# Kernel tuning notes

Measured on AMD Instinct MI355X. Metric: run time of the kernel, lower is better.

## Reference

```python
import jax, jax.numpy as jnp
import numpy as np

NEG_SLOPE = 0.2  # PyG GATConv default leaky_relu slope
BN_EPS = 1e-5


def gat_conv(x, src, dst, num_nodes, W, a_src, a_dst, bias, concat):
    """PyG-style GATConv (eval mode, self-loops already appended to src/dst)."""
    H, F = a_src.shape
    h = (x @ W).reshape(num_nodes, H, F)              # [N,H,F]
    e_src = jnp.einsum('nhf,hf->nh', h, a_src)        # [N,H]
    e_dst = jnp.einsum('nhf,hf->nh', h, a_dst)        # [N,H]
    e = jax.nn.leaky_relu(e_src[src] + e_dst[dst], NEG_SLOPE)  # [E,H]
    m = jax.ops.segment_max(e, dst, num_segments=num_nodes)    # segment softmax (stable)
    w = jnp.exp(e - m[dst])
    z = jax.ops.segment_sum(w, dst, num_segments=num_nodes)
    alpha = w / (z[dst] + 1e-16)                      # [E,H]
    msg = alpha[:, :, None] * h[src]                  # [E,H,F]
    out = jax.ops.segment_sum(msg, dst, num_segments=num_nodes)  # [N,H,F]
    out = out.reshape(num_nodes, H * F) if concat else out.mean(axis=1)
    return out + bias


def bn_eval(x, gamma, beta):
    # BatchNorm1d eval with initialized running stats (mean=0, var=1)
    return x * (gamma / jnp.sqrt(1.0 + BN_EPS)) + beta


def setup_inputs() -> dict:
    key = jax.random.key(0)
    ks = jax.random.split(key, 16)
    N, E, Fin, H, Fh, MLP = 50000, 800000, 128, 4, 32, 64
    HF = H * Fh  # 128
    s = 0.05
    inp = {
        'x': jax.random.normal(ks[0], (N, Fin), jnp.float32),
        'edge_index': jax.random.randint(ks[1], (2, E), 0, N, jnp.int64),
        # conv0: Fin -> Fh per head, concat
        'W1': jax.random.normal(ks[2], (Fin, HF), jnp.float32) * s,
        'a1s': jax.random.normal(ks[3], (H, Fh), jnp.float32) * s,
        'a1d': jax.random.normal(ks[4], (H, Fh), jnp.float32) * s,
        'b1': jnp.zeros((HF,), jnp.float32),
        # conv1: HF -> Fh per head, concat
        'W2': jax.random.normal(ks[5], (HF, HF), jnp.float32) * s,
        'a2s': jax.random.normal(ks[6], (H, Fh), jnp.float32) * s,
        'a2d': jax.random.normal(ks[7], (H, Fh), jnp.float32) * s,
        'b2': jnp.zeros((HF,), jnp.float32),
        # mlp block 0
        'M1w': jax.random.normal(ks[8], (HF, MLP), jnp.float32) * s,
        'M1b': jnp.zeros((MLP,), jnp.float32),
        'g1': jnp.ones((MLP,), jnp.float32),
        'be1': jnp.zeros((MLP,), jnp.float32),
        'M2w': jax.random.normal(ks[9], (MLP, HF), jnp.float32) * s,
        'M2b': jnp.zeros((HF,), jnp.float32),
        'g2': jnp.ones((HF,), jnp.float32),
        'be2': jnp.zeros((HF,), jnp.float32),
        # conv2: HF -> Fh per head, mean over heads (concat=False)
        'W3': jax.random.normal(ks[10], (HF, HF), jnp.float32) * s,
        'a3s': jax.random.normal(ks[11], (H, Fh), jnp.float32) * s,
        'a3d': jax.random.normal(ks[12], (H, Fh), jnp.float32) * s,
        'b3': jnp.zeros((Fh,), jnp.float32),
    }
    return inp


def reference(x, edge_index, W1, a1s, a1d, b1, W2, a2s, a2d, b2,
              M1w, M1b, g1, be1, M2w, M2b, g2, be2, W3, a3s, a3d, b3):
    N = x.shape[0]
    loops = jnp.arange(N, dtype=edge_index.dtype)
    src = jnp.concatenate([edge_index[0], loops])  # add self-loops (PyG default)
    dst = jnp.concatenate([edge_index[1], loops])

    # layer 0: conv -> relu -> (dropout=id, eval) -> mlp[0]
    h = jax.nn.relu(gat_conv(x, src, dst, N, W1, a1s, a1d, b1, concat=True))
    h = bn_eval(jax.nn.relu(h @ M1w + M1b), g1, be1)
    h = bn_eval(jax.nn.relu(h @ M2w + M2b), g2, be2)

    # layer 1: conv -> relu -> (dropout=id)
    h = jax.nn.relu(gat_conv(h, src, dst, N, W2, a2s, a2d, b2, concat=True))

    # output layer: concat=False -> mean over heads
    out = gat_conv(h, src, dst, N, W3, a3s, a3d, b3, concat=False)
    return out
```

## Files before the change

### kernel.cpp

```cpp
#include <hip/hip_runtime.h>
#include <hip/hip_bf16.h>

#define NEG_SLOPE 0.2f
#define BN_RS 0.9999950000374997f

typedef __attribute__((ext_vector_type(8))) _Float16 f16x8;
typedef __attribute__((ext_vector_type(2))) _Float16 f16x2;
typedef __attribute__((ext_vector_type(4))) float f32x4;

__device__ __forceinline__ void store_split(float w, _Float16* H, _Float16* L, size_t off) {
  _Float16 h = (_Float16)w;
  H[off] = h;
  L[off] = (_Float16)(w - (float)h);
}


__global__ void zero256(int* p) { p[threadIdx.x] = 0; }

__global__ void eb_hist(const int* __restrict__ ei, int* __restrict__ bucketSize, int E) {
  __shared__ int h[256];
  int tid = threadIdx.x;
  h[tid] = 0;
  __syncthreads();
  for (int i = blockIdx.x * 256 + tid; i < E; i += gridDim.x * 256)
    atomicAdd(&h[ei[E + i] >> 8], 1);
  __syncthreads();
  if (h[tid]) atomicAdd(&bucketSize[tid], h[tid]);
}

__global__ void eb_scan(const int* __restrict__ bucketSize, int* __restrict__ edgeStart,
                        int* __restrict__ cursor, int* __restrict__ csrStart, int N) {
  __shared__ int sd[256];
  int tid = threadIdx.x;
  int v = bucketSize[tid];
  sd[tid] = v;
  __syncthreads();
  for (int off = 1; off < 256; off <<= 1) {
    int t = (tid >= off) ? sd[tid - off] : 0;
    __syncthreads();
    sd[tid] += t;
    __syncthreads();
  }
  int excl = sd[tid] - v;
  edgeStart[tid] = excl;
  cursor[tid] = excl;
  csrStart[tid] = excl + min(tid << 8, N);
  if (tid == 255) edgeStart[256] = sd[255];
}

#define PCH 4096
__global__ __launch_bounds__(256) void eb_part(const int* __restrict__ ei,
                                               int* __restrict__ cursor,
                                               unsigned* __restrict__ staging, int E) {
  __shared__ unsigned val[PCH];
  __shared__ unsigned char bk[PCH];
  __shared__ int cnt[256];
  __shared__ int base[256];
  int tid = threadIdx.x;
  cnt[tid] = 0;
  __syncthreads();
  int e0 = blockIdx.x * PCH;
  int n = min(PCH, E - e0);
  for (int j = tid; j < n; j += 256) {
    int s = ei[e0 + j], d = ei[E + e0 + j];
    val[j] = ((unsigned)(d & 255) << 16) | (unsigned)s;
    int b = d >> 8;
    bk[j] = (unsigned char)b;
    atomicAdd(&cnt[b], 1);
  }
  __syncthreads();
  if (cnt[tid]) base[tid] = atomicAdd(&cursor[tid], cnt[tid]);
  __syncthreads();
  for (int j = tid; j < n; j += 256) {
    int b = bk[j];
    int off = atomicSub(&cnt[b], 1) - 1;
    staging[base[b] + off] = val[j];
  }
}

__global__ __launch_bounds__(256) void eb_csr(
    const unsigned* __restrict__ staging, const int* __restrict__ edgeStart,
    const int* __restrict__ csrStart, int* __restrict__ rowptr,
    unsigned* __restrict__ csr, int N) {
  __shared__ int deg[256];
  __shared__ int sc[256];
  __shared__ int ex[256];
  int b = blockIdx.x, tid = threadIdx.x;
  int n0 = b << 8;
  int nn = min(256, N - n0);
  deg[tid] = (tid < nn) ? 1 : 0;
  __syncthreads();
  int s0 = edgeStart[b], s1 = edgeStart[b + 1];
  for (int j = s0 + tid; j < s1; j += 256)
    atomicAdd(&deg[staging[j] >> 16], 1);
  __syncthreads();
  int dv = deg[tid];
  sc[tid] = dv;
  __syncthreads();
  for (int off = 1; off < 256; off <<= 1) {
    int t = (tid >= off) ? sc[tid - off] : 0;
    __syncthreads();
    sc[tid] += t;
    __syncthreads();
  }
  int incl = sc[tid];
  int cbase = csrStart[b];
  ex[tid] = incl - dv;
  if (tid < nn) {
    rowptr[n0 + tid + 1] = cbase + incl;
    unsigned me = (unsigned)(n0 + tid);
    csr[cbase + incl - 1] = (me << 16) | me;
  }
  if (b == 0 && tid == 0) rowptr[0] = 0;
  deg[tid] = 0;
  __syncthreads();
  for (int j = s0 + tid; j < s1; j += 256) {
    unsigned v = staging[j];
    int dl = v >> 16;
    unsigned src = v & 0xFFFF;
    int off = atomicAdd(&deg[dl], 1);
    csr[cbase + ex[dl] + off] = ((unsigned)(n0 + dl) << 16) | src;
  }
}

__device__ __forceinline__ void wprep_conv(const float* __restrict__ W,
                                           const float* __restrict__ as_,
                                           const float* __restrict__ ad_,
                                           _Float16* __restrict__ H, _Float16* __restrict__ L,
                                           int lb, int tid) {
  if (lb < 64) {
    int idx = lb * 256 + tid;
    int k = idx >> 7, p = idx & 127;
    store_split(W[k * 128 + p], H, L, (size_t)p * 128 + k);
  } else if (lb < 68) {
    int idx = (lb - 64) * 256 + tid;
    int rl = idx >> 7, k = idx & 127;
    const float* a = (rl < 4) ? as_ : ad_;
    int h = rl & 3;
    float s = 0.f;
#pragma unroll
    for (int f = 0; f < 32; f++) s += W[k * 128 + h * 32 + f] * a[h * 32 + f];
    store_split(s, H, L, (size_t)(128 + rl) * 128 + k);
  } else {
    int idx = (lb - 68) * 256 + tid;
    int rl = idx >> 7, k = idx & 127;
    H[(size_t)(136 + rl) * 128 + k] = (_Float16)0.f;
    L[(size_t)(136 + rl) * 128 + k] = (_Float16)0.f;
  }
}

__global__ void wprep_all(
    const float* __restrict__ W1, const float* __restrict__ a1s, const float* __restrict__ a1d,
    _Float16* __restrict__ W1H, _Float16* __restrict__ W1L,
    const float* __restrict__ W2, const float* __restrict__ a2s, const float* __restrict__ a2d,
    _Float16* __restrict__ W2H, _Float16* __restrict__ W2L,
    const float* __restrict__ W3, const float* __restrict__ a3s, const float* __restrict__ a3d,
    _Float16* __restrict__ W3H, _Float16* __restrict__ W3L,
    const float* __restrict__ M1, _Float16* __restrict__ M1H, _Float16* __restrict__ M1L,
    const float* __restrict__ M2, _Float16* __restrict__ M2H, _Float16* __restrict__ M2L) {
  int b = blockIdx.x, tid = threadIdx.x;
  if (b < 72)       wprep_conv(W1, a1s, a1d, W1H, W1L, b, tid);
  else if (b < 144) wprep_conv(W2, a2s, a2d, W2H, W2L, b - 72, tid);
  else if (b < 216) wprep_conv(W3, a3s, a3d, W3H, W3L, b - 144, tid);
  else if (b < 248) {
    int idx = (b - 216) * 256 + tid;
    int k = idx >> 6, p = idx & 63;
    store_split(M1[k * 64 + p], M1H, M1L, (size_t)p * 128 + k);
  } else {
    int idx = (b - 248) * 256 + tid;
    int k = idx >> 7, p = idx & 127;
    store_split(M2[k * 128 + p], M2H, M2L, (size_t)p * 64 + k);
  }
}

template <typename TA>
__global__ __launch_bounds__(256) void gemm_f16(
    const TA* __restrict__ A, const _Float16* __restrict__ WtH,
    const _Float16* __restrict__ WtL, _Float16* __restrict__ C, int N,
    float* __restrict__ esb, float* __restrict__ edb) {
  constexpr int PT = 144, PST = 128, K = 128;
  constexpr int CTB = 2;
  constexpr int KT = K / 32;
  __shared__ _Float16 As[128 * 32];
  __shared__ _Float16 WsH[PT * 32];
  __shared__ _Float16 WsL[PT * 32];
  const int tid = threadIdx.x;
  const int wave = tid >> 6, lane = tid & 63;
  const int quad = lane >> 4, l16 = lane & 15;
  const int row0 = blockIdx.x * 128;
  const bool xw = (wave == 0);

  f32x4 acc[8][CTB + 1];
#pragma unroll
  for (int rt = 0; rt < 8; rt++)
#pragma unroll
    for (int nt = 0; nt < CTB + 1; nt++) acc[rt][nt] = (f32x4){0.f, 0.f, 0.f, 0.f};

  for (int kc = 0; kc < KT; ++kc) {
    {
      int r = tid >> 1, part = tid & 1;
      int gr = row0 + r;
      _Float16* dst = &As[r * 32 + part * 16];
      if (gr < N) {
        const TA* src = A + (size_t)gr * K + kc * 32 + part * 16;
        if constexpr (sizeof(TA) == 4) {
          f16x8 h0, h1;
#pragma unroll
          for (int j = 0; j < 8; j++) { h0[j] = (_Float16)src[j]; h1[j] = (_Float16)src[8 + j]; }
          *(f16x8*)dst = h0; *(f16x8*)(dst + 8) = h1;
        } else {
          uint4 v0 = *(const uint4*)src;
          uint4 v1 = *(const uint4*)(src + 8);
          *(uint4*)dst = v0; *(uint4*)(dst + 8) = v1;
        }
      } else {
        *(uint4*)dst = make_uint4(0, 0, 0, 0);
        *(uint4*)(dst + 8) = make_uint4(0, 0, 0, 0);
      }
    }
    for (int idx = tid; idx < PT * 2; idx += 256) {
      int isL = idx >= PT;
      int p = isL ? idx - PT : idx;
      const _Float16* src = (isL ? WtL : WtH) + (size_t)p * K + kc * 32;
      _Float16* dst = (isL ? WsL : WsH) + p * 32;
      uint4 a0 = *(const uint4*)src;       uint4 a1 = *(const uint4*)(src + 8);
      uint4 a2 = *(const uint4*)(src + 16); uint4 a3 = *(const uint4*)(src + 24);
      *(uint4*)dst = a0; *(uint4*)(dst + 8) = a1;
      *(uint4*)(dst + 16) = a2; *(uint4*)(dst + 24) = a3;
    }
    __syncthreads();

    f16x8 bh[CTB], bl[CTB], bhE, blE;
#pragma unroll
    for (int nt = 0; nt < CTB; nt++) {
      int p = (wave * CTB + nt) * 16 + l16;
      bh[nt] = *(f16x8*)&WsH[p * 32 + quad * 8];
      bl[nt] = *(f16x8*)&WsL[p * 32 + quad * 8];
    }
    if (xw) {
      int p = 4 * CTB * 16 + l16;
      bhE = *(f16x8*)&WsH[p * 32 + quad * 8];
      blE = *(f16x8*)&WsL[p * 32 + quad * 8];
    }
#pragma unroll
    for (int rt = 0; rt < 8; rt++) {
      f16x8 a = *(f16x8*)&As[(rt * 16 + l16) * 32 + quad * 8];
#pragma unroll
      for (int nt = 0; nt < CTB; nt++) {
        acc[rt][nt] = __builtin_amdgcn_mfma_f32_16x16x32_f16(a, bh[nt], acc[rt][nt], 0, 0, 0);
        acc[rt][nt] = __builtin_amdgcn_mfma_f32_16x16x32_f16(a, bl[nt], acc[rt][nt], 0, 0, 0);
      }
      if (xw) {
        acc[rt][CTB] = __builtin_amdgcn_mfma_f32_16x16x32_f16(a, bhE, acc[rt][CTB], 0, 0, 0);
        acc[rt][CTB] = __builtin_amdgcn_mfma_f32_16x16x32_f16(a, blE, acc[rt][CTB], 0, 0, 0);
      }
    }
    __syncthreads();
  }

#pragma unroll
  for (int nt = 0; nt < CTB; nt++) {
    int c = (wave * CTB + nt) * 16 + l16;
#pragma unroll
    for (int rt = 0; rt < 8; rt++)
#pragma unroll
      for (int g = 0; g < 4; g++) {
        int r = row0 + rt * 16 + quad * 4 + g;
        if (r < N) C[(size_t)r * PST + c] = (_Float16)acc[rt][nt][g];
      }
  }
  if (wave == 0 && l16 < 8) {
    float* dstb = (l16 < 4) ? esb : edb;
    int h = l16 & 3;
#pragma unroll
    for (int rt = 0; rt < 8; rt++)
#pragma unroll
      for (int g = 0; g < 4; g++) {
        int r = row0 + rt * 16 + quad * 4 + g;
        if (r < N) dstb[(size_t)r * 4 + h] = acc[rt][CTB][g];
      }
  }
}

__global__ __launch_bounds__(256) void mlp_fused(
    const _Float16* __restrict__ A,
    const _Float16* __restrict__ M1H, const _Float16* __restrict__ M1L,
    const _Float16* __restrict__ M2H, const _Float16* __restrict__ M2L,
    _Float16* __restrict__ C, int N,
    const float* __restrict__ b1v, const float* __restrict__ g1v, const float* __restrict__ be1v,
    const float* __restrict__ b2v, const float* __restrict__ g2v, const float* __restrict__ be2v) {
  __shared__ _Float16 As[128 * 32];
  __shared__ _Float16 W1Hs[64 * 32], W1Ls[64 * 32];
  __shared__ _Float16 T[128 * 72];
  __shared__ _Float16 W2Hs[128 * 32], W2Ls[128 * 32];
  const int tid = threadIdx.x;
  const int wave = tid >> 6, lane = tid & 63;
  const int quad = lane >> 4, l16 = lane & 15;
  const int row0 = blockIdx.x * 128;

  f32x4 acc1[8];
#pragma unroll
  for (int rt = 0; rt < 8; rt++) acc1[rt] = (f32x4){0.f, 0.f, 0.f, 0.f};
  for (int kc = 0; kc < 4; ++kc) {
    {
      int r = tid >> 1, part = tid & 1;
      int gr = row0 + r;
      _Float16* dst = &As[r * 32 + part * 16];
      if (gr < N) {
        const _Float16* src = A + (size_t)gr * 128 + kc * 32 + part * 16;
        uint4 v0 = *(const uint4*)src;
        uint4 v1 = *(const uint4*)(src + 8);
        *(uint4*)dst = v0; *(uint4*)(dst + 8) = v1;
      } else {
        *(uint4*)dst = make_uint4(0, 0, 0, 0);
        *(uint4*)(dst + 8) = make_uint4(0, 0, 0, 0);
      }
    }
    if (tid < 128) {
      int isL = tid >= 64;
      int p = tid & 63;
      const _Float16* src = (isL ? M1L : M1H) + (size_t)p * 128 + kc * 32;
      _Float16* dst = (isL ? W1Ls : W1Hs) + p * 32;
      uint4 a0 = *(const uint4*)src;       uint4 a1 = *(const uint4*)(src + 8);
      uint4 a2 = *(const uint4*)(src + 16); uint4 a3 = *(const uint4*)(src + 24);
      *(uint4*)dst = a0; *(uint4*)(dst + 8) = a1;
      *(uint4*)(dst + 16) = a2; *(uint4*)(dst + 24) = a3;
    }
    __syncthreads();
    int p = wave * 16 + l16;
    f16x8 bh = *(f16x8*)&W1Hs[p * 32 + quad * 8];
    f16x8 bl = *(f16x8*)&W1Ls[p * 32 + quad * 8];
#pragma unroll
    for (int rt = 0; rt < 8; rt++) {
      f16x8 a = *(f16x8*)&As[(rt * 16 + l16) * 32 + quad * 8];
      acc1[rt] = __builtin_amdgcn_mfma_f32_16x16x32_f16(a, bh, acc1[rt], 0, 0, 0);
      acc1[rt] = __builtin_amdgcn_mfma_f32_16x16x32_f16(a, bl, acc1[rt], 0, 0, 0);
    }
    __syncthreads();
  }
  {
    int c = wave * 16 + l16;
    float bi = b1v[c], ga = g1v[c] * BN_RS, be = be1v[c];
#pragma unroll
    for (int rt = 0; rt < 8; rt++)
#pragma unroll
      for (int g = 0; g < 4; g++) {
        int r = rt * 16 + quad * 4 + g;
        float v = acc1[rt][g] + bi;
        v = v > 0.f ? v : 0.f;
        v = v * ga + be;
        T[r * 72 + c] = (_Float16)v;
      }
  }
  __syncthreads();

  f32x4 acc2[8][2];
#pragma unroll
  for (int rt = 0; rt < 8; rt++)
#pragma unroll
    for (int nt = 0; nt < 2; nt++) acc2[rt][nt] = (f32x4){0.f, 0.f, 0.f, 0.f};
  for (int kc = 0; kc < 2; ++kc) {
    {
      int isL = tid >= 128;
      int p = tid & 127;
      const _Float16* src = (isL ? M2L : M2H) + (size_t)p * 64 + kc * 32;
      _Float16* dst = (isL ? W2Ls : W2Hs) + p * 32;
      uint4 a0 = *(const uint4*)src;       uint4 a1 = *(const uint4*)(src + 8);
      uint4 a2 = *(const uint4*)(src + 16); uint4 a3 = *(const uint4*)(src + 24);
      *(uint4*)dst = a0; *(uint4*)(dst + 8) = a1;
      *(uint4*)(dst + 16) = a2; *(uint4*)(dst + 24) = a3;
    }
    __syncthreads();
    f16x8 bh[2], bl[2];
#pragma unroll
    for (int nt = 0; nt < 2; nt++) {
      int p = (wave * 2 + nt) * 16 + l16;
      bh[nt] = *(f16x8*)&W2Hs[p * 32 + quad * 8];
      bl[nt] = *(f16x8*)&W2Ls[p * 32 + quad * 8];
    }
#pragma unroll
    for (int rt = 0; rt < 8; rt++) {
      f16x8 a = *(f16x8*)&T[(rt * 16 + l16) * 72 + kc * 32 + quad * 8];
#pragma unroll
      for (int nt = 0; nt < 2; nt++) {
        acc2[rt][nt] = __builtin_amdgcn_mfma_f32_16x16x32_f16(a, bh[nt], acc2[rt][nt], 0, 0, 0);
        acc2[rt][nt] = __builtin_amdgcn_mfma_f32_16x16x32_f16(a, bl[nt], acc2[rt][nt], 0, 0, 0);
      }
    }
    __syncthreads();
  }
#pragma unroll
  for (int nt = 0; nt < 2; nt++) {
    int c = (wave * 2 + nt) * 16 + l16;
    float bi = b2v[c], ga = g2v[c] * BN_RS, be = be2v[c];
#pragma unroll
    for (int rt = 0; rt < 8; rt++)
#pragma unroll
      for (int g = 0; g < 4; g++) {
        int r = row0 + rt * 16 + quad * 4 + g;
        if (r < N) {
          float v = acc2[rt][nt][g] + bi;
          v = v > 0.f ? v : 0.f;
          v = v * ga + be;
          C[(size_t)r * 128 + c] = (_Float16)v;
        }
      }
  }
}

template <int MODE>
__global__ __launch_bounds__(256) void gat_agg(
    const _Float16* __restrict__ hx, const int* __restrict__ rowptr,
    const unsigned* __restrict__ csr, const float* __restrict__ es,
    const float* __restrict__ ed, const float* __restrict__ bias,
    void* __restrict__ outp, int N) {
  __shared__ float wbuf[4][2][16][4];
  __shared__ int sbuf[4][2][16];
  int wid = __builtin_amdgcn_readfirstlane((int)((blockIdx.x * 256 + threadIdx.x) >> 6));
  if (wid >= N) return;
  int wave = threadIdx.x >> 6;
  int lane = threadIdx.x & 63;
  int head = lane >> 4;
  int j4 = lane >> 2, h4 = lane & 3;
  int beg = rowptr[wid], end = rowptr[wid + 1];
  float edv4 = ed[wid * 4 + h4];
  float ax = 0.f, ay = 0.f, z = 0.f;
  const _Float16* hb = hx + 2 * lane;
  int nch = (end - beg + 15) >> 4;

  {
    int m = end - beg; if (m > 16) m = 16;
    if (j4 < m) {
      int s = (int)(csr[beg + j4] & 0xFFFFu);
      float t = es[s * 4 + h4] + edv4;
      t = t > 0.f ? t : NEG_SLOPE * t;
      wbuf[wave][0][j4][h4] = __expf(t);
      if (h4 == 0) sbuf[wave][0][j4] = s;
    }
  }
  int pb = 0;
  for (int ci = 0; ci < nch; ++ci) {
    int c = beg + (ci << 4);
    int m = end - c; if (m > 16) m = 16;
    if (ci + 1 < nch) {
      int c2 = c + 16;
      int m2 = end - c2; if (m2 > 16) m2 = 16;
      if (j4 < m2) {
        int s = (int)(csr[c2 + j4] & 0xFFFFu);
        float t = es[s * 4 + h4] + edv4;
        t = t > 0.f ? t : NEG_SLOPE * t;
        wbuf[wave][pb ^ 1][j4][h4] = __expf(t);
        if (h4 == 0) sbuf[wave][pb ^ 1][j4] = s;
      }
    }
    int j = 0;
    for (; j + 8 <= m; j += 8) {
      int s0 = sbuf[wave][pb][j + 0], s1 = sbuf[wave][pb][j + 1];
      int s2 = sbuf[wave][pb][j + 2], s3 = sbuf[wave][pb][j + 3];
      int s4 = sbuf[wave][pb][j + 4], s5 = sbuf[wave][pb][j + 5];
      int s6 = sbuf[wave][pb][j + 6], s7 = sbuf[wave][pb][j + 7];
      float w0 = wbuf[wave][pb][j + 0][head], w1 = wbuf[wave][pb][j + 1][head];
      float w2 = wbuf[wave][pb][j + 2][head], w3 = wbuf[wave][pb][j + 3][head];
      float w4 = wbuf[wave][pb][j + 4][head], w5 = wbuf[wave][pb][j + 5][head];
      float w6 = wbuf[wave][pb][j + 6][head], w7 = wbuf[wave][pb][j + 7][head];
      f16x2 h0 = *(const f16x2*)(hb + (size_t)s0 * 128);
      f16x2 h1 = *(const f16x2*)(hb + (size_t)s1 * 128);
      f16x2 h2 = *(const f16x2*)(hb + (size_t)s2 * 128);
      f16x2 h3 = *(const f16x2*)(hb + (size_t)s3 * 128);
      f16x2 h4v = *(const f16x2*)(hb + (size_t)s4 * 128);
      f16x2 h5 = *(const f16x2*)(hb + (size_t)s5 * 128);
      f16x2 h6 = *(const f16x2*)(hb + (size_t)s6 * 128);
      f16x2 h7 = *(const f16x2*)(hb + (size_t)s7 * 128);
      z += ((w0 + w1) + (w2 + w3)) + ((w4 + w5) + (w6 + w7));
      ax = fmaf(w0, (float)h0[0], ax); ay = fmaf(w0, (float)h0[1], ay);
      ax = fmaf(w1, (float)h1[0], ax); ay = fmaf(w1, (float)h1[1], ay);
      ax = fmaf(w2, (float)h2[0], ax); ay = fmaf(w2, (float)h2[1], ay);
      ax = fmaf(w3, (float)h3[0], ax); ay = fmaf(w3, (float)h3[1], ay);
      ax = fmaf(w4, (float)h4v[0], ax); ay = fmaf(w4, (float)h4v[1], ay);
      ax = fmaf(w5, (float)h5[0], ax); ay = fmaf(w5, (float)h5[1], ay);
      ax = fmaf(w6, (float)h6[0], ax); ay = fmaf(w6, (float)h6[1], ay);
      ax = fmaf(w7, (float)h7[0], ax); ay = fmaf(w7, (float)h7[1], ay);
    }
    for (; j < m; ++j) {
      int s = sbuf[wave][pb][j];
      float w = wbuf[wave][pb][j][head];
      f16x2 hv = *(const f16x2*)(hb + (size_t)s * 128);
      z += w;
      ax = fmaf(w, (float)hv[0], ax);
      ay = fmaf(w, (float)hv[1], ay);
    }
    pb ^= 1;
  }
  float inv = 1.f / (z + 1e-16f);
  float vx = ax * inv, vy = ay * inv;
  if (MODE == 0) {
    vx += bias[2 * lane]; vy += bias[2 * lane + 1];
    vx = vx > 0.f ? vx : 0.f;  vy = vy > 0.f ? vy : 0.f;
    f16x2 o; o[0] = (_Float16)vx; o[1] = (_Float16)vy;
    *(f16x2*)((_Float16*)outp + (size_t)wid * 128 + 2 * lane) = o;
  } else {
    vx += __shfl_xor(vx, 16); vx += __shfl_xor(vx, 32);
    vy += __shfl_xor(vy, 16); vy += __shfl_xor(vy, 32);
    if (lane < 16) {
      float ox = vx * 0.25f + bias[2 * lane];
      float oy = vy * 0.25f + bias[2 * lane + 1];
      *(float2*)((float*)outp + (size_t)wid * 32 + 2 * lane) = make_float2(ox, oy);
    }
  }
}

extern "C" void kernel_launch(void* const* d_in, const int* in_sizes, int n_in,
                              void* d_out, int out_size, void* d_ws, size_t ws_size,
                              hipStream_t stream) {
  const float* x   = (const float*)d_in[0];
  const int*   ei  = (const int*)d_in[1];
  const float* W1  = (const float*)d_in[2];
  const float* a1s = (const float*)d_in[3];
  const float* a1d = (const float*)d_in[4];
  const float* b1  = (const float*)d_in[5];
  const float* W2  = (const float*)d_in[6];
  const float* a2s = (const float*)d_in[7];
  const float* a2d = (const float*)d_in[8];
  const float* b2  = (const float*)d_in[9];
  const float* M1w = (const float*)d_in[10];
  const float* M1b = (const float*)d_in[11];
  const float* g1  = (const float*)d_in[12];
  const float* be1 = (const float*)d_in[13];
  const float* M2w = (const float*)d_in[14];
  const float* M2b = (const float*)d_in[15];
  const float* g2  = (const float*)d_in[16];
  const float* be2 = (const float*)d_in[17];
  const float* W3  = (const float*)d_in[18];
  const float* a3s = (const float*)d_in[19];
  const float* a3d = (const float*)d_in[20];
  const float* b3  = (const float*)d_in[21];

  const int N = in_sizes[0] / 128;
  const int E = in_sizes[1] / 2;
  const int S = E + N;

  char* w = (char*)d_ws;
  _Float16* bufA = (_Float16*)w; w += (size_t)N * 128 * 2;
  _Float16* bufB = (_Float16*)w; w += (size_t)N * 128 * 2;
  float* esb  = (float*)w; w += (size_t)N * 4 * 4;
  float* edb  = (float*)w; w += (size_t)N * 4 * 4;
  int* rowptr = (int*)w;   w += (size_t)(N + 1) * 4;
  unsigned* csr = (unsigned*)w; w += (size_t)S * 4;
  unsigned* staging = (unsigned*)w; w += (size_t)E * 4;
  int* bucketSize = (int*)w; w += 256 * 4;
  int* edgeStart  = (int*)w; w += 257 * 4;
  int* cursor     = (int*)w; w += 256 * 4;
  int* csrStart   = (int*)w; w += 256 * 4;
  _Float16* W1H = (_Float16*)w; w += 144 * 128 * 2;
  _Float16* W1L = (_Float16*)w; w += 144 * 128 * 2;
  _Float16* W2H = (_Float16*)w; w += 144 * 128 * 2;
  _Float16* W2L = (_Float16*)w; w += 144 * 128 * 2;
  _Float16* W3H = (_Float16*)w; w += 144 * 128 * 2;
  _Float16* W3L = (_Float16*)w; w += 144 * 128 * 2;
  _Float16* M1H = (_Float16*)w; w += 64 * 128 * 2;
  _Float16* M1L = (_Float16*)w; w += 64 * 128 * 2;
  _Float16* M2H = (_Float16*)w; w += 128 * 64 * 2;
  _Float16* M2L = (_Float16*)w; w += 128 * 64 * 2;

  const int gb = (N + 127) / 128;
  const int aggb = (N + 3) / 4;
  const int nbk = (N + 255) / 256;
  const int pbk = (E + PCH - 1) / PCH;

  wprep_all<<<280, 256, 0, stream>>>(W1, a1s, a1d, W1H, W1L,
                                     W2, a2s, a2d, W2H, W2L,
                                     W3, a3s, a3d, W3H, W3L,
                                     M1w, M1H, M1L, M2w, M2H, M2L);

  zero256<<<1, 256, 0, stream>>>(bucketSize);
  eb_hist<<<256, 256, 0, stream>>>(ei, bucketSize, E);
  eb_scan<<<1, 256, 0, stream>>>(bucketSize, edgeStart, cursor, csrStart, N);
  eb_part<<<pbk, 256, 0, stream>>>(ei, cursor, staging, E);
  eb_csr<<<nbk, 256, 0, stream>>>(staging, edgeStart, csrStart, rowptr, csr, N);

  gemm_f16<float><<<gb, 256, 0, stream>>>(x, W1H, W1L, bufA, N, esb, edb);
  gat_agg<0><<<aggb, 256, 0, stream>>>(bufA, rowptr, csr, esb, edb, b1, bufB, N);
  mlp_fused<<<gb, 256, 0, stream>>>(bufB, M1H, M1L, M2H, M2L, bufA, N,
                                    M1b, g1, be1, M2b, g2, be2);

  gemm_f16<_Float16><<<gb, 256, 0, stream>>>(bufA, W2H, W2L, bufB, N, esb, edb);
  gat_agg<0><<<aggb, 256, 0, stream>>>(bufB, rowptr, csr, esb, edb, b2, bufA, N);

  gemm_f16<_Float16><<<gb, 256, 0, stream>>>(bufA, W3H, W3L, bufB, N, esb, edb);
  gat_agg<1><<<aggb, 256, 0, stream>>>(bufB, rowptr, csr, esb, edb, b3, d_out, N);
}
```

Baseline: 336.8 us.

## Aggregate four nodes per wave with 16-byte feature gathers; fold bucket zeroing

The GAT aggregation kernel now processes four destination nodes per wavefront, with 16 lanes per node. Each lane gathers eight fp16 features per neighbor in one 16-byte load instead of two, and attention logits are read as a float4 per edge, cutting the number of narrow gathers. The separate bucket-zeroing launch is folded into the weight-prep kernel as an extra block, saving one launch. The trade-off is more registers per lane, and more divergence when nodes sharing a wave have very different degrees.

```diff
diff --git a/kernel.cpp b/kernel.cpp
--- a/kernel.cpp
+++ b/kernel.cpp
@@ -14,8 +14,6 @@
   L[off] = (_Float16)(w - (float)h);
 }
 
-
-__global__ void zero256(int* p) { p[threadIdx.x] = 0; }
 
 __global__ void eb_hist(const int* __restrict__ ei, int* __restrict__ bucketSize, int E) {
   __shared__ int h[256];
@@ -157,7 +155,8 @@
     const float* __restrict__ W3, const float* __restrict__ a3s, const float* __restrict__ a3d,
     _Float16* __restrict__ W3H, _Float16* __restrict__ W3L,
     const float* __restrict__ M1, _Float16* __restrict__ M1H, _Float16* __restrict__ M1L,
-    const float* __restrict__ M2, _Float16* __restrict__ M2H, _Float16* __restrict__ M2L) {
+    const float* __restrict__ M2, _Float16* __restrict__ M2H, _Float16* __restrict__ M2L,
+    int* __restrict__ bucketSize) {
   int b = blockIdx.x, tid = threadIdx.x;
   if (b < 72)       wprep_conv(W1, a1s, a1d, W1H, W1L, b, tid);
   else if (b < 144) wprep_conv(W2, a2s, a2d, W2H, W2L, b - 72, tid);
@@ -166,10 +165,12 @@
     int idx = (b - 216) * 256 + tid;
     int k = idx >> 6, p = idx & 63;
     store_split(M1[k * 64 + p], M1H, M1L, (size_t)p * 128 + k);
-  } else {
+  } else if (b < 280) {
     int idx = (b - 248) * 256 + tid;
     int k = idx >> 7, p = idx & 127;
     store_split(M2[k * 128 + p], M2H, M2L, (size_t)p * 64 + k);
+  } else {
+    bucketSize[tid] = 0;
   }
 }
 
@@ -414,28 +415,38 @@
     const unsigned* __restrict__ csr, const float* __restrict__ es,
     const float* __restrict__ ed, const float* __restrict__ bias,
     void* __restrict__ outp, int N) {
-  __shared__ float wbuf[4][2][16][4];
-  __shared__ int sbuf[4][2][16];
-  int wid = __builtin_amdgcn_readfirstlane((int)((blockIdx.x * 256 + threadIdx.x) >> 6));
-  if (wid >= N) return;
-  int wave = threadIdx.x >> 6;
-  int lane = threadIdx.x & 63;
-  int head = lane >> 4;
-  int j4 = lane >> 2, h4 = lane & 3;
-  int beg = rowptr[wid], end = rowptr[wid + 1];
-  float edv4 = ed[wid * 4 + h4];
-  float ax = 0.f, ay = 0.f, z = 0.f;
-  const _Float16* hb = hx + 2 * lane;
-  int nch = (end - beg + 15) >> 4;
+  __shared__ float4 wbuf[4][4][2][17];
+  __shared__ int    sbuf[4][4][2][16];
+  const int tid = threadIdx.x;
+  const int wave = tid >> 6, lane = tid & 63;
+  const int g = lane >> 4, il = lane & 15;
+  const int hd = il >> 2;
+  const int nid = (blockIdx.x * 4 + wave) * 4 + g;
+  const bool valid = (nid < N);
+  int beg = 0, end = 0;
+  if (valid) { beg = rowptr[nid]; end = rowptr[nid + 1]; }
+  float4 edv = make_float4(0.f, 0.f, 0.f, 0.f);
+  if (valid) edv = *(const float4*)(ed + (size_t)nid * 4);
+  float acc[8];
+#pragma unroll
+  for (int r = 0; r < 8; r++) acc[r] = 0.f;
+  float z = 0.f;
+  const _Float16* hb = hx + il * 8;
+  const int nch = (end - beg + 15) >> 4;
 
   {
     int m = end - beg; if (m > 16) m = 16;
-    if (j4 < m) {
-      int s = (int)(csr[beg + j4] & 0xFFFFu);
-      float t = es[s * 4 + h4] + edv4;
-      t = t > 0.f ? t : NEG_SLOPE * t;
-      wbuf[wave][0][j4][h4] = __expf(t);
-      if (h4 == 0) sbuf[wave][0][j4] = s;
+    if (il < m) {
+      int s = (int)(csr[beg + il] & 0xFFFFu);
+      float4 e4 = *(const float4*)(es + (size_t)s * 4);
+      float t0 = e4.x + edv.x, t1 = e4.y + edv.y;
+      float t2 = e4.z + edv.z, t3 = e4.w + edv.w;
+      t0 = t0 > 0.f ? t0 : NEG_SLOPE * t0;
+      t1 = t1 > 0.f ? t1 : NEG_SLOPE * t1;
+      t2 = t2 > 0.f ? t2 : NEG_SLOPE * t2;
+      t3 = t3 > 0.f ? t3 : NEG_SLOPE * t3;
+      wbuf[wave][g][0][il] = make_float4(__expf(t0), __expf(t1), __expf(t2), __expf(t3));
+      sbuf[wave][g][0][il] = s;
     }
   }
   int pb = 0;
@@ -445,66 +456,82 @@
     if (ci + 1 < nch) {
       int c2 = c + 16;
       int m2 = end - c2; if (m2 > 16) m2 = 16;
-      if (j4 < m2) {
-        int s = (int)(csr[c2 + j4] & 0xFFFFu);
-        float t = es[s * 4 + h4] + edv4;
-        t = t > 0.f ? t : NEG_SLOPE * t;
-        wbuf[wave][pb ^ 1][j4][h4] = __expf(t);
-        if (h4 == 0) sbuf[wave][pb ^ 1][j4] = s;
-      }
-    }
+      if (il < m2) {
+        int s = (int)(csr[c2 + il] & 0xFFFFu);
+        float4 e4 = *(const float4*)(es + (size_t)s * 4);
+        float t0 = e4.x + edv.x, t1 = e4.y + edv.y;
+        float t2 = e4.z + edv.z, t3 = e4.w + edv.w;
+        t0 = t0 > 0.f ? t0 : NEG_SLOPE * t0;
+        t1 = t1 > 0.f ? t1 : NEG_SLOPE * t1;
+        t2 = t2 > 0.f ? t2 : NEG_SLOPE * t2;
+        t3 = t3 > 0.f ? t3 : NEG_SLOPE * t3;
+        wbuf[wave][g][pb ^ 1][il] = make_float4(__expf(t0), __expf(t1), __expf(t2), __expf(t3));
+        sbuf[wave][g][pb ^ 1][il] = s;
+      }
+    }
+    const float* wp = (const float*)&wbuf[wave][g][pb][0];
+    const int*   sp = &sbuf[wave][g][pb][0];
     int j = 0;
-    for (; j + 8 <= m; j += 8) {
-      int s0 = sbuf[wave][pb][j + 0], s1 = sbuf[wave][pb][j + 1];
-      int s2 = sbuf[wave][pb][j + 2], s3 = sbuf[wave][pb][j + 3];
-      int s4 = sbuf[wave][pb][j + 4], s5 = sbuf[wave][pb][j + 5];
-      int s6 = sbuf[wave][pb][j + 6], s7 = sbuf[wave][pb][j + 7];
-      float w0 = wbuf[wave][pb][j + 0][head], w1 = wbuf[wave][pb][j + 1][head];
-      float w2 = wbuf[wave][pb][j + 2][head], w3 = wbuf[wave][pb][j + 3][head];
-      float w4 = wbuf[wave][pb][j + 4][head], w5 = wbuf[wave][pb][j + 5][head];
-      float w6 = wbuf[wave][pb][j + 6][head], w7 = wbuf[wave][pb][j + 7][head];
-      f16x2 h0 = *(const f16x2*)(hb + (size_t)s0 * 128);
-      f16x2 h1 = *(const f16x2*)(hb + (size_t)s1 * 128);
-      f16x2 h2 = *(const f16x2*)(hb + (size_t)s2 * 128);
-      f16x2 h3 = *(const f16x2*)(hb + (size_t)s3 * 128);
-      f16x2 h4v = *(const f16x2*)(hb + (size_t)s4 * 128);
-      f16x2 h5 = *(const f16x2*)(hb + (size_t)s5 * 128);
-      f16x2 h6 = *(const f16x2*)(hb + (size_t)s6 * 128);
-      f16x2 h7 = *(const f16x2*)(hb + (size_t)s7 * 128);
-      z += ((w0 + w1) + (w2 + w3)) + ((w4 + w5) + (w6 + w7));
-      ax = fmaf(w0, (float)h0[0], ax); ay = fmaf(w0, (float)h0[1], ay);
-      ax = fmaf(w1, (float)h1[0], ax); ay = fmaf(w1, (float)h1[1], ay);
-      ax = fmaf(w2, (float)h2[0], ax); ay = fmaf(w2, (float)h2[1], ay);
-      ax = fmaf(w3, (float)h3[0], ax); ay = fmaf(w3, (float)h3[1], ay);
-      ax = fmaf(w4, (float)h4v[0], ax); ay = fmaf(w4, (float)h4v[1], ay);
-      ax = fmaf(w5, (float)h5[0], ax); ay = fmaf(w5, (float)h5[1], ay);
-      ax = fmaf(w6, (float)h6[0], ax); ay = fmaf(w6, (float)h6[1], ay);
-      ax = fmaf(w7, (float)h7[0], ax); ay = fmaf(w7, (float)h7[1], ay);
+    for (; j + 4 <= m; j += 4) {
+      int s0 = sp[j], s1 = sp[j + 1], s2 = sp[j + 2], s3 = sp[j + 3];
+      float w0 = wp[(j + 0) * 4 + hd], w1 = wp[(j + 1) * 4 + hd];
+      float w2 = wp[(j + 2) * 4 + hd], w3 = wp[(j + 3) * 4 + hd];
+      f16x8 r0 = *(const f16x8*)(hb + (size_t)s0 * 128);
+      f16x8 r1 = *(const f16x8*)(hb + (size_t)s1 * 128);
+      f16x8 r2 = *(const f16x8*)(hb + (size_t)s2 * 128);
+      f16x8 r3 = *(const f16x8*)(hb + (size_t)s3 * 128);
+      z += (w0 + w1) + (w2 + w3);
+#pragma unroll
+      for (int r = 0; r < 8; r++) {
+        float a = acc[r];
+        a = fmaf(w0, (float)r0[r], a);
+        a = fmaf(w1, (float)r1[r], a);
+        a = fmaf(w2, (float)r2[r], a);
+        a = fmaf(w3, (float)r3[r], a);
+        acc[r] = a;
+      }
     }
     for (; j < m; ++j) {
-      int s = sbuf[wave][pb][j];
-      float w = wbuf[wave][pb][j][head];
-      f16x2 hv = *(const f16x2*)(hb + (size_t)s * 128);
+      int s = sp[j];
+      float w = wp[j * 4 + hd];
+      f16x8 rv = *(const f16x8*)(hb + (size_t)s * 128);
       z += w;
-      ax = fmaf(w, (float)hv[0], ax);
-      ay = fmaf(w, (float)hv[1], ay);
+#pragma unroll
+      for (int r = 0; r < 8; r++) acc[r] = fmaf(w, (float)rv[r], acc[r]);
     }
     pb ^= 1;
   }
   float inv = 1.f / (z + 1e-16f);
-  float vx = ax * inv, vy = ay * inv;
   if (MODE == 0) {
-    vx += bias[2 * lane]; vy += bias[2 * lane + 1];
-    vx = vx > 0.f ? vx : 0.f;  vy = vy > 0.f ? vy : 0.f;
-    f16x2 o; o[0] = (_Float16)vx; o[1] = (_Float16)vy;
-    *(f16x2*)((_Float16*)outp + (size_t)wid * 128 + 2 * lane) = o;
+    f16x8 o;
+#pragma unroll
+    for (int r = 0; r < 8; r++) {
+      float v = acc[r] * inv + bias[il * 8 + r];
+      v = v > 0.f ? v : 0.f;
+      o[r] = (_Float16)v;
+    }
+    if (valid) *(f16x8*)((_Float16*)outp + (size_t)nid * 128 + il * 8) = o;
   } else {
-    vx += __shfl_xor(vx, 16); vx += __shfl_xor(vx, 32);
-    vy += __shfl_xor(vy, 16); vy += __shfl_xor(vy, 32);
-    if (lane < 16) {
-      float ox = vx * 0.25f + bias[2 * lane];
-      float oy = vy * 0.25f + bias[2 * lane + 1];
-      *(float2*)((float*)outp + (size_t)wid * 32 + 2 * lane) = make_float2(ox, oy);
+    float v[8];
+#pragma unroll
+    for (int r = 0; r < 8; r++) {
+      float t = acc[r] * inv;
+      t += __shfl_xor(t, 4);
+      t += __shfl_xor(t, 8);
+      v[r] = t;
+    }
+    if (valid && il < 4) {
+      float4 o0, o1;
+      o0.x = v[0] * 0.25f + bias[il * 8 + 0];
+      o0.y = v[1] * 0.25f + bias[il * 8 + 1];
+      o0.z = v[2] * 0.25f + bias[il * 8 + 2];
+      o0.w = v[3] * 0.25f + bias[il * 8 + 3];
+      o1.x = v[4] * 0.25f + bias[il * 8 + 4];
+      o1.y = v[5] * 0.25f + bias[il * 8 + 5];
+      o1.z = v[6] * 0.25f + bias[il * 8 + 6];
+      o1.w = v[7] * 0.25f + bias[il * 8 + 7];
+      *(float4*)((float*)outp + (size_t)nid * 32 + il * 8) = o0;
+      *(float4*)((float*)outp + (size_t)nid * 32 + il * 8 + 4) = o1;
     }
   }
 }
@@ -563,16 +590,15 @@
   _Float16* M2L = (_Float16*)w; w += 128 * 64 * 2;
 
   const int gb = (N + 127) / 128;
-  const int aggb = (N + 3) / 4;
+  const int aggb = (N + 15) / 16;
   const int nbk = (N + 255) / 256;
   const int pbk = (E + PCH - 1) / PCH;
 
-  wprep_all<<<280, 256, 0, stream>>>(W1, a1s, a1d, W1H, W1L,
+  wprep_all<<<281, 256, 0, stream>>>(W1, a1s, a1d, W1H, W1L,
                                      W2, a2s, a2d, W2H, W2L,
                                      W3, a3s, a3d, W3H, W3L,
-                                     M1w, M1H, M1L, M2w, M2H, M2L);
-
-  zero256<<<1, 256, 0, stream>>>(bucketSize);
+                                     M1w, M1H, M1L, M2w, M2H, M2L, bucketSize);
+
   eb_hist<<<256, 256, 0, stream>>>(ei, bucketSize, E);
   eb_scan<<<1, 256, 0, stream>>>(bucketSize, edgeStart, cursor, csrStart, N);
   eb_part<<<pbk, 256, 0, stream>>>(ei, cursor, staging, E);
```

Result: faster. 322.6 us, median of 2 (-4.2%).
